# Kernel tuning notes

Hardware: AMD Instinct MI355X
Metric: run time of the kernel (lower is better)

## Reference

```python
import jax, jax.numpy as jnp
import numpy as np

DIM = 256
NUM_HEADS = 8
HEAD_DIM = DIM // NUM_HEADS  # 32
SCALE = HEAD_DIM ** (-0.5)


def _conv1x1(x, w, b):
    # x: [B,C,H,W], w: [O,C,1,1], b: [O]
    return jnp.einsum('bchw,oc->bohw', x, w[:, :, 0, 0]) + b[None, :, None, None]


def _dwconv3x3(x, w, b):
    # depthwise conv, groups=C, padding=1 (SAME)
    y = jax.lax.conv_general_dilated(
        x, w, window_strides=(1, 1), padding='SAME',
        feature_group_count=x.shape[1],
        dimension_numbers=('NCHW', 'OIHW', 'NCHW'))
    return y + b[None, :, None, None]


def setup_inputs() -> dict:
    key = jax.random.key(0)
    ks = jax.random.split(key, 9)
    s = 0.05
    return {
        'x': jax.random.normal(ks[0], (4, DIM, 48, 48), jnp.float32),
        'w_qk': jax.random.normal(ks[1], (2 * DIM, DIM, 1, 1), jnp.float32) * s,
        'b_qk': jax.random.normal(ks[2], (2 * DIM,), jnp.float32) * s,
        'w_v': jax.random.normal(ks[3], (DIM, DIM, 1, 1), jnp.float32) * s,
        'b_v': jax.random.normal(ks[4], (DIM,), jnp.float32) * s,
        'w_pe': jax.random.normal(ks[5], (DIM, 1, 3, 3), jnp.float32) * s,
        'b_pe': jax.random.normal(ks[6], (DIM,), jnp.float32) * s,
        'w_proj': jax.random.normal(ks[7], (DIM, DIM, 1, 1), jnp.float32) * s,
        'b_proj': jax.random.normal(ks[8], (DIM,), jnp.float32) * s,
    }


def reference(x, w_qk, b_qk, w_v, b_v, w_pe, b_pe, w_proj, b_proj):
    B, C, H, W = x.shape
    N = H * W
    h, d = NUM_HEADS, HEAD_DIM

    qk = _conv1x1(x, w_qk, b_qk).reshape(B, h, 2 * d, N)
    v4 = _conv1x1(x, w_v, b_v)                # [B,C,H,W]
    pe = _dwconv3x3(v4, w_pe, b_pe)           # [B,C,H,W]
    v = v4.reshape(B, h, d, N)

    q, k = qk[:, :, :d, :], qk[:, :, d:, :]   # [B,h,d,N] each
    attn = jnp.einsum('bhdi,bhdj->bhij', q, k) * SCALE  # [B,h,N,N]
    attn = jax.nn.softmax(attn, axis=-1)
    out = jnp.einsum('bhdj,bhij->bhdi', v, attn)        # [B,h,d,N]
    out = out.reshape(B, C, H, W)

    return _conv1x1(out + pe, w_proj, b_proj)
```

## Files before the change

### kernel.cpp

```cpp
#include <hip/hip_runtime.h>
#include <hip/hip_bf16.h>

#define NPIX 2304
#define HW 48
#define CDIM 256
#define NHEADS 8
#define HD 32
#define SCALE_CONST 0.17677669529663687f
#define LOG2E 1.4426950408889634f

typedef __attribute__((ext_vector_type(8))) short  short8v;
typedef __attribute__((ext_vector_type(4))) short  short4v;
typedef __attribute__((ext_vector_type(4))) float  floatx4;

__device__ inline short f2bf(float f) {
    unsigned u = __builtin_bit_cast(unsigned, f);
    u += 0x7FFFu + ((u >> 16) & 1u);
    return (short)(u >> 16);
}
__device__ inline float bf2f(unsigned short us) {
    return __builtin_bit_cast(float, (unsigned)us << 16);
}
__device__ inline float fexp2(float x) {
    return __builtin_amdgcn_exp2f(x);
}

__global__ __launch_bounds__(256) void prep_kernel(
    const float* __restrict__ x,
    short* __restrict__ XT,
    const float* __restrict__ wqk, const float* __restrict__ wv,
    const float* __restrict__ wp,
    short* __restrict__ wqkb, short* __restrict__ wvb, short* __restrict__ wpb)
{
    const int bx = blockIdx.x;
    const int t = threadIdx.x;
    if (bx >= 576) {
        int tid = (bx - 576) * 256 + t;
        for (int idx = tid; idx < 262144; idx += 16384) {
            if (idx < 131072)       wqkb[idx] = f2bf(wqk[idx]);
            else if (idx < 196608)  wvb[idx - 131072] = f2bf(wv[idx - 131072]);
            else                    wpb[idx - 196608] = f2bf(wp[idx - 196608]);
        }
        return;
    }
    __shared__ float sT[64][65];
    const int nt = bx % 36, ct = (bx / 36) & 3, b = bx / 144;
    const int c0 = ct * 64, n0 = nt * 64;
    const float* sp = x + ((size_t)b * 256 + c0) * NPIX + n0;
    const int cl = t >> 6, n = t & 63;
#pragma unroll
    for (int it = 0; it < 16; ++it) {
        int c = it * 4 + cl;
        sT[n][c] = sp[(size_t)c * NPIX + n];
    }
    __syncthreads();
    const int nr = t >> 2, q = t & 3;
    short out[16];
#pragma unroll
    for (int j = 0; j < 16; ++j) out[j] = f2bf(sT[nr][q * 16 + j]);
    short* dp = XT + ((size_t)b * NPIX + n0 + nr) * 256 + c0 + q * 16;
    *(int4*)dp = *(int4*)out;
    *(int4*)(dp + 8) = *(int4*)(out + 8);
}

#define XROW 528

__device__ inline void stage_xt_tile(const short* __restrict__ src_base,
                                     char* __restrict__ sX, int t)
{
    const short* src = src_base + (size_t)(t >> 3) * 256 + (t & 7) * 32;
    char* dst = sX + (t >> 3) * XROW + (t & 7) * 64;
#pragma unroll
    for (int rr = 0; rr < 2; ++rr) {
        const short* s = src + rr * 32 * 256;
        char* d = dst + rr * 32 * XROW;
        *(int4*)d        = *(const int4*)s;
        *(int4*)(d + 16) = *(const int4*)(s + 8);
        *(int4*)(d + 32) = *(const int4*)(s + 16);
        *(int4*)(d + 48) = *(const int4*)(s + 24);
    }
}

__global__ __launch_bounds__(256) void conv_qkv_mfma(
    const short* __restrict__ Wqk,
    const short* __restrict__ Wv,
    const float* __restrict__ bqk,
    const float* __restrict__ bv,
    const short* __restrict__ XT,
    short* __restrict__ QT,
    short* __restrict__ KT,
    short* __restrict__ VB)
{
    __shared__ __align__(16) char sX[64 * XROW];
    const int xcd = blockIdx.x & 7;
    const int loc = blockIdx.x >> 3;
    const int yy  = loc % 6;
    const int T   = (loc / 6) * 8 + xcd;
    const int n0  = (T % 36) * 64;
    const int b   = T / 36;

    const int t = threadIdx.x, lane = t & 63, w = t >> 6;
    const int l15 = lane & 15, quad = lane >> 4;

    stage_xt_tile(XT + ((size_t)b * NPIX + n0) * 256, sX, t);
    __syncthreads();

    floatx4 accs[2][4];
#pragma unroll
    for (int g = 0; g < 2; ++g) {
        const int og = yy + g * 6;
        const bool isV = (og >= 8);
        const short* Wb = isV ? Wv + (size_t)((og - 8) * 64 + w * 16 + l15) * CDIM
                              : Wqk + (size_t)(og * 64 + w * 16 + l15) * CDIM;
        short8v afv[8];
#pragma unroll
        for (int s = 0; s < 8; ++s)
            afv[s] = *(const short8v*)(Wb + s * 32 + quad * 8);
#pragma unroll
        for (int ib = 0; ib < 4; ++ib) accs[g][ib] = (floatx4){0.f, 0.f, 0.f, 0.f};
#pragma unroll
        for (int s = 0; s < 8; ++s) {
#pragma unroll
            for (int ib = 0; ib < 4; ++ib) {
                short8v bf = *(const short8v*)(sX + (ib * 16 + l15) * XROW + s * 64 + quad * 16);
                accs[g][ib] = __builtin_amdgcn_mfma_f32_16x16x32_bf16(afv[s], bf, accs[g][ib], 0, 0, 0);
            }
        }
    }

#pragma unroll
    for (int g = 0; g < 2; ++g) {
        const int og = yy + g * 6;
        const bool isV = (og >= 8);
        __syncthreads();
        if (!isV) {
            const bool isQ = (w < 2);
            const float scl = isQ ? SCALE_CONST * LOG2E : 1.0f;
            float bvv[4];
#pragma unroll
            for (int r = 0; r < 4; ++r) bvv[r] = bqk[og * 64 + w * 16 + quad * 4 + r];
#pragma unroll
            for (int ib = 0; ib < 4; ++ib) {
                short pb[4];
#pragma unroll
                for (int r = 0; r < 4; ++r) pb[r] = f2bf((accs[g][ib][r] + bvv[r]) * scl);
                *(short4v*)(sX + (ib * 16 + l15) * 136 + (w * 16 + quad * 4) * 2) = *(short4v*)pb;
            }
            __syncthreads();
            const int n = t >> 2, q = t & 3;
            int4 v0 = *(const int4*)(sX + n * 136 + q * 32);
            int4 v1 = *(const int4*)(sX + n * 136 + q * 32 + 16);
            short* dst = ((q < 2) ? QT : KT)
                       + ((size_t)(b * 8 + og) * NPIX + n0 + n) * HD + (q & 1) * 16;
            *(int4*)dst = v0;
            *(int4*)(dst + 8) = v1;
        } else {
            const int o0 = (og - 8) * 64 + w * 16 + quad * 4;
            float bvv[4];
#pragma unroll
            for (int r = 0; r < 4; ++r) bvv[r] = bv[o0 + r];
#pragma unroll
            for (int ib = 0; ib < 4; ++ib) {
                short pb[4];
#pragma unroll
                for (int r = 0; r < 4; ++r) pb[r] = f2bf(accs[g][ib][r] + bvv[r]);
                *(short4v*)(sX + (ib * 16 + l15) * 132 + (w * 16 + quad * 4) * 2) = *(short4v*)pb;
            }
            __syncthreads();
            const int o = t >> 2, q = t & 3;
            short tmp[16];
#pragma unroll
            for (int k = 0; k < 16; ++k)
                tmp[k] = *(const short*)(sX + (q * 16 + k) * 132 + o * 2);
            short* dst = VB + ((size_t)b * 256 + (og - 8) * 64 + o) * NPIX + n0 + q * 16;
            *(int4*)dst = *(int4*)tmp;
            *(int4*)(dst + 8) = *(int4*)(tmp + 8);
        }
    }
}

#define KROW 72
#define VROW 136
#define PROW 136
#define SK0 0
#define SK1 4608
#define SV0 9216
#define SV1 13568
#define SP0 17920
#define FL_SMEM 26624
#define DROW 170

__global__ __launch_bounds__(256) void flash_attn_mfma(
    const short* __restrict__ QT,
    const short* __restrict__ KT,
    const short* __restrict__ VB,
    const float* __restrict__ w_pe,
    const float* __restrict__ b_pe,
    short* __restrict__ ST)
{
    __shared__ __align__(16) char smem[FL_SMEM];

    const int hh   = blockIdx.x & 7;
    const int slot = blockIdx.x >> 3;
    const int b    = slot / 36;
    const int i0   = (slot % 36) * 64;
    const int bh   = b * 8 + hh;

    const short* KTp = KT + (size_t)bh * NPIX * HD;
    const short* Vp  = VB + (size_t)(b * 256 + hh * HD) * NPIX;

    const int t    = threadIdx.x;
    const int lane = t & 63;
    const int w    = t >> 6;
    const int l15  = lane & 15;
    const int quad = lane >> 4;

    const short8v qfrag = *(const short8v*)(
        QT + ((size_t)bh * NPIX + i0 + w * 16 + l15) * HD + quad * 8);

    short8v ones;
#pragma unroll
    for (int k = 0; k < 8; ++k) ones[k] = (short)0x3F80;

    char* const sPw = smem + SP0 + w * (16 * PROW);

    floatx4 oacc[2], lacc;
    oacc[0] = (floatx4){0.f, 0.f, 0.f, 0.f};
    oacc[1] = (floatx4){0.f, 0.f, 0.f, 0.f};
    lacc    = (floatx4){0.f, 0.f, 0.f, 0.f};

    const short* ksrc = KTp + (size_t)(t >> 2) * HD + (t & 3) * 8;
    const short* vsrc = Vp + (size_t)(t >> 3) * NPIX + (t & 7) * 8;
    const int koff = (t >> 2) * KROW + (t & 3) * 16;
    const int voff = (t >> 3) * VROW + (t & 7) * 16;

    int4 kst = *(const int4*)ksrc;
    int4 vst = *(const int4*)vsrc;

    for (int it = 0; it < 36; ++it) {
        char* bufK = smem + ((it & 1) ? SK1 : SK0);
        char* bufV = smem + ((it & 1) ? SV1 : SV0);
        *(int2*)(bufK + koff)     = *(int2*)&kst;
        *(int2*)(bufK + koff + 8) = *((int2*)&kst + 1);
        *(int2*)(bufV + voff)     = *(int2*)&vst;
        *(int2*)(bufV + voff + 8) = *((int2*)&vst + 1);
        if (it + 1 < 36) {
            kst = *(const int4*)(ksrc + (size_t)(it + 1) * 64 * HD);
            vst = *(const int4*)(vsrc + (it + 1) * 64);
        }
        __syncthreads();

        floatx4 sacc[4];
#pragma unroll
        for (int jb = 0; jb < 4; ++jb) {
            const char* ka = bufK + (jb * 16 + l15) * KROW + quad * 16;
            short8v af;
            ((int2*)&af)[0] = *(const int2*)ka;
            ((int2*)&af)[1] = *(const int2*)(ka + 8);
            sacc[jb] = __builtin_amdgcn_mfma_f32_16x16x32_bf16(
                af, qfrag, (floatx4){0.f, 0.f, 0.f, 0.f}, 0, 0, 0);
        }

#pragma unroll
        for (int jb = 0; jb < 4; ++jb) {
            unsigned tb[4];
#pragma unroll
            for (int r = 0; r < 4; ++r)
                tb[r] = __builtin_bit_cast(unsigned, fexp2(sacc[jb][r]));
            int2 pw;
            pw.x = (int)__builtin_amdgcn_perm(tb[1], tb[0], 0x07060302u);
            pw.y = (int)__builtin_amdgcn_perm(tb[3], tb[2], 0x07060302u);
            *(int2*)(sPw + l15 * PROW + jb * 32 + quad * 8) = pw;
        }

#pragma unroll
        for (int ks = 0; ks < 2; ++ks) {
            const char* pa = sPw + l15 * PROW + ks * 64 + quad * 16;
            short8v pf;
            ((int2*)&pf)[0] = *(const int2*)pa;
            ((int2*)&pf)[1] = *(const int2*)(pa + 8);
#pragma unroll
            for (int db = 0; db < 2; ++db) {
                const char* va = bufV + (db * 16 + l15) * VROW + ks * 64 + quad * 16;
                short8v vf;
                ((int2*)&vf)[0] = *(const int2*)va;
                ((int2*)&vf)[1] = *(const int2*)(va + 8);
                oacc[db] = __builtin_amdgcn_mfma_f32_16x16x32_bf16(vf, pf, oacc[db], 0, 0, 0);
            }
            lacc = __builtin_amdgcn_mfma_f32_16x16x32_bf16(ones, pf, lacc, 0, 0, 0);
        }
    }

    const float invl = 1.0f / lacc[0];
    __syncthreads();

    short* const sO    = (short*)smem;
    short* const sHalo = (short*)(smem + 4608);

    {
        const int il = w * 16 + l15;
#pragma unroll
        for (int db = 0; db < 2; ++db) {
            short ob[4];
#pragma unroll
            for (int r = 0; r < 4; ++r) ob[r] = f2bf(oacc[db][r] * invl);
            *(short4v*)(sO + il * 36 + db * 16 + quad * 4) = *(short4v*)ob;
        }
    }
    for (int ch8 = t; ch8 < 672; ch8 += 256) {
        int ch = ch8 / 21, off = (ch8 % 21) * 8;
        int base = i0 - 52 + off;
        const short* src = VB + ((size_t)b * 256 + hh * HD + ch) * NPIX;
        short tmp[8];
        if (base >= 0 && base + 8 <= NPIX) {
            *(int4*)tmp = *(const int4*)(src + base);
        } else {
#pragma unroll
            for (int u = 0; u < 8; ++u) {
                int p = base + u;
                tmp[u] = (p >= 0 && p < NPIX) ? src[p] : (short)0;
            }
        }
        *(int4*)&sHalo[ch * DROW + off] = *(int4*)tmp;
    }
    __syncthreads();

    {
        const int d  = t & 31;
        const int pg = t >> 5;
        const int c  = hh * HD + d;
        float wv[9];
#pragma unroll
        for (int k = 0; k < 9; ++k) wv[k] = w_pe[c * 9 + k];
        const float bb = b_pe[c];
        const int px0  = i0 + pg * 8;
        const int col0 = px0 % HW;
        const short* sprow = &sHalo[d * DROW + 52 + pg * 8];
        short* stp = ST + ((size_t)b * NPIX + px0) * 256 + c;

#pragma unroll
        for (int u = 0; u < 8; ++u) {
            int colu = col0 + u; if (colu >= HW) colu -= HW;
            const bool okL = (colu != 0), okR = (colu != HW - 1);
            float a = bb;
#pragma unroll
            for (int dy = 0; dy < 3; ++dy) {
                int ci = u + (dy - 1) * HW;
                a += wv[dy * 3 + 1] * bf2f((unsigned short)sprow[ci]);
                if (okL) a += wv[dy * 3 + 0] * bf2f((unsigned short)sprow[ci - 1]);
                if (okR) a += wv[dy * 3 + 2] * bf2f((unsigned short)sprow[ci + 1]);
            }
            float o = bf2f((unsigned short)sO[(pg * 8 + u) * 36 + d]);
            stp[(size_t)u * 256] = f2bf(o + a);
        }
    }
}

__global__ __launch_bounds__(256) void conv_proj_mfma(
    const short* __restrict__ Wb,
    const float* __restrict__ bias,
    const short* __restrict__ ST,
    float* __restrict__ out)
{
    __shared__ __align__(16) char sX[64 * XROW];
    const int xcd = blockIdx.x & 7;
    const int loc = blockIdx.x >> 3;
    const int og  = loc % 4;
    const int T   = (loc / 4) * 8 + xcd;
    const int n0  = (T % 36) * 64;
    const int b   = T / 36;

    const int t = threadIdx.x, lane = t & 63, w = t >> 6;
    const int l15 = lane & 15, quad = lane >> 4;

    stage_xt_tile(ST + ((size_t)b * NPIX + n0) * 256, sX, t);

    const short* Arow = Wb + (size_t)(og * 64 + w * 16 + l15) * CDIM;
    short8v afv[8];
#pragma unroll
    for (int s = 0; s < 8; ++s)
        afv[s] = *(const short8v*)(Arow + s * 32 + quad * 8);

    __syncthreads();

    floatx4 acc[4];
#pragma unroll
    for (int ib = 0; ib < 4; ++ib) acc[ib] = (floatx4){0.f, 0.f, 0.f, 0.f};
#pragma unroll
    for (int s = 0; s < 8; ++s) {
#pragma unroll
        for (int ib = 0; ib < 4; ++ib) {
            short8v bf = *(const short8v*)(sX + (ib * 16 + l15) * XROW + s * 64 + quad * 16);
            acc[ib] = __builtin_amdgcn_mfma_f32_16x16x32_bf16(afv[s], bf, acc[ib], 0, 0, 0);
        }
    }
    __syncthreads();

    {
        float bvv[4];
#pragma unroll
        for (int r = 0; r < 4; ++r) bvv[r] = bias[og * 64 + w * 16 + quad * 4 + r];
        float* sRep = (float*)sX;
#pragma unroll
        for (int r = 0; r < 4; ++r)
#pragma unroll
            for (int ib = 0; ib < 4; ++ib)
                sRep[(w * 16 + quad * 4 + r) * 68 + ib * 16 + l15] = acc[ib][r] + bvv[r];
    }
    __syncthreads();

    const int o = t >> 2, q = t & 3;
    const float* src = (const float*)sX + o * 68 + q * 16;
    float* dst = out + ((size_t)b * 256 + og * 64 + o) * NPIX + n0 + q * 16;
#pragma unroll
    for (int k = 0; k < 4; ++k)
        *(int4*)(dst + k * 4) = *(const int4*)(src + k * 4);
}

extern "C" void kernel_launch(void* const* d_in, const int* in_sizes, int n_in,
                              void* d_out, int out_size, void* d_ws, size_t ws_size,
                              hipStream_t stream) {
    const float* x      = (const float*)d_in[0];
    const float* w_qk   = (const float*)d_in[1];
    const float* b_qk   = (const float*)d_in[2];
    const float* w_v    = (const float*)d_in[3];
    const float* b_v    = (const float*)d_in[4];
    const float* w_pe   = (const float*)d_in[5];
    const float* b_pe   = (const float*)d_in[6];
    const float* w_proj = (const float*)d_in[7];
    const float* b_proj = (const float*)d_in[8];
    float* out = (float*)d_out;

    char* wsb = (char*)d_ws;
    short* ws_xt  = (short*)wsb;  wsb += (size_t)4 * NPIX * 256 * 2;
    short* ws_qt  = (short*)wsb;  wsb += (size_t)32 * NPIX * HD * 2;
    short* ws_kt  = (short*)wsb;  wsb += (size_t)32 * NPIX * HD * 2;
    short* ws_vb  = (short*)wsb;  wsb += (size_t)4 * 256 * NPIX * 2;
    short* ws_st  = (short*)wsb;  wsb += (size_t)4 * NPIX * 256 * 2;
    short* ws_wqk = (short*)wsb;  wsb += (size_t)512 * 256 * 2;
    short* ws_wv  = (short*)wsb;  wsb += (size_t)256 * 256 * 2;
    short* ws_wp  = (short*)wsb;  wsb += (size_t)256 * 256 * 2;

    prep_kernel<<<dim3(640), 256, 0, stream>>>(x, ws_xt, w_qk, w_v, w_proj,
                                               ws_wqk, ws_wv, ws_wp);
    conv_qkv_mfma<<<dim3(864), 256, 0, stream>>>(ws_wqk, ws_wv, b_qk, b_v,
                                                 ws_xt, ws_qt, ws_kt, ws_vb);
    flash_attn_mfma<<<dim3(1152), 256, 0, stream>>>(ws_qt, ws_kt, ws_vb,
                                                    w_pe, b_pe, ws_st);
    conv_proj_mfma<<<dim3(576), 256, 0, stream>>>(ws_wp, b_proj, ws_st, out);
}
```

Measured before the change: 157.9 us.

## Load K/V MFMA fragments directly from global instead of staging through LDS

Removes the double-buffered shared-memory staging of K and V tiles and the per-iteration block barrier. Each wave now reads its MFMA operand fragments straight from global memory (served by L1/L2), and shared memory shrinks to the P scratch and epilogue buffers. This drops the LDS writes and syncs and may raise occupancy. In exchange, each of the four waves issues its own redundant global loads of the same K/V data, and there is no software prefetch to hide their latency.

After: 227.4 us. 1.44x slower.

```diff
diff --git a/kernel.cpp b/kernel.cpp
--- a/kernel.cpp
+++ b/kernel.cpp
@@ -179,15 +179,9 @@
     }
 }
 
-#define KROW 72
-#define VROW 136
 #define PROW 136
-#define SK0 0
-#define SK1 4608
-#define SV0 9216
-#define SV1 13568
-#define SP0 17920
-#define FL_SMEM 26624
+#define SP0 0
+#define FL_SMEM 15488
 #define DROW 170
 
 __global__ __launch_bounds__(256) void flash_attn_mfma(
@@ -229,34 +223,16 @@
     oacc[1] = (floatx4){0.f, 0.f, 0.f, 0.f};
     lacc    = (floatx4){0.f, 0.f, 0.f, 0.f};
 
-    const short* ksrc = KTp + (size_t)(t >> 2) * HD + (t & 3) * 8;
-    const short* vsrc = Vp + (size_t)(t >> 3) * NPIX + (t & 7) * 8;
-    const int koff = (t >> 2) * KROW + (t & 3) * 16;
-    const int voff = (t >> 3) * VROW + (t & 7) * 16;
-
-    int4 kst = *(const int4*)ksrc;
-    int4 vst = *(const int4*)vsrc;
+    const short* kfp = KTp + (size_t)l15 * HD + quad * 8;
+    const short* vfp = Vp + (size_t)l15 * NPIX + quad * 8;
 
     for (int it = 0; it < 36; ++it) {
-        char* bufK = smem + ((it & 1) ? SK1 : SK0);
-        char* bufV = smem + ((it & 1) ? SV1 : SV0);
-        *(int2*)(bufK + koff)     = *(int2*)&kst;
-        *(int2*)(bufK + koff + 8) = *((int2*)&kst + 1);
-        *(int2*)(bufV + voff)     = *(int2*)&vst;
-        *(int2*)(bufV + voff + 8) = *((int2*)&vst + 1);
-        if (it + 1 < 36) {
-            kst = *(const int4*)(ksrc + (size_t)(it + 1) * 64 * HD);
-            vst = *(const int4*)(vsrc + (it + 1) * 64);
-        }
-        __syncthreads();
+        const int j0 = it * 64;
 
         floatx4 sacc[4];
 #pragma unroll
         for (int jb = 0; jb < 4; ++jb) {
-            const char* ka = bufK + (jb * 16 + l15) * KROW + quad * 16;
-            short8v af;
-            ((int2*)&af)[0] = *(const int2*)ka;
-            ((int2*)&af)[1] = *(const int2*)(ka + 8);
+            short8v af = *(const short8v*)(kfp + (size_t)(j0 + jb * 16) * HD);
             sacc[jb] = __builtin_amdgcn_mfma_f32_16x16x32_bf16(
                 af, qfrag, (floatx4){0.f, 0.f, 0.f, 0.f}, 0, 0, 0);
         }
@@ -281,10 +257,8 @@
             ((int2*)&pf)[1] = *(const int2*)(pa + 8);
 #pragma unroll
             for (int db = 0; db < 2; ++db) {
-                const char* va = bufV + (db * 16 + l15) * VROW + ks * 64 + quad * 16;
-                short8v vf;
-                ((int2*)&vf)[0] = *(const int2*)va;
-                ((int2*)&vf)[1] = *(const int2*)(va + 8);
+                short8v vf = *(const short8v*)(
+                    vfp + (size_t)(db * 16) * NPIX + j0 + ks * 32);
                 oacc[db] = __builtin_amdgcn_mfma_f32_16x16x32_bf16(vf, pf, oacc[db], 0, 0, 0);
             }
             lacc = __builtin_amdgcn_mfma_f32_16x16x32_bf16(ones, pf, lacc, 0, 0, 0);
```
